# Optimization experiments

Measured on AMD Instinct MI355X. Metric: run time of the kernel, lower is better.

## Reference

```python
import jax, jax.numpy as jnp
import numpy as np
from jax import lax

B, C, H, W = 2, 384, 32, 32
N_HEAD, N_GROUP = 12, 6
HC = C // N_HEAD          # 32 head channels
GC = C // N_GROUP         # 64 group channels
GH = N_HEAD // N_GROUP    # 2 heads per group
KK = 7                    # depthwise kernel (25<=32<=48)
OFF_FACTOR = 2.0
SCALE = HC ** -0.5
EPS = 1e-5


def setup_inputs() -> dict:
    key = jax.random.key(0)
    ks = jax.random.split(key, 16)
    s = 0.02
    inp = {
        "x": jax.random.normal(ks[0], (B, C, H, W), jnp.float32),
        "Wq": jax.random.normal(ks[1], (C, C), jnp.float32) * s,
        "bq": jnp.zeros((C,), jnp.float32),
        "Wk": jax.random.normal(ks[2], (C, C), jnp.float32) * s,
        "bk": jnp.zeros((C,), jnp.float32),
        "Wv": jax.random.normal(ks[3], (C, C), jnp.float32) * s,
        "bv": jnp.zeros((C,), jnp.float32),
        "Wo": jax.random.normal(ks[4], (C, C), jnp.float32) * s,
        "bo": jnp.zeros((C,), jnp.float32),
        "off_dw_w": jax.random.normal(ks[5], (GC, 1, KK, KK), jnp.float32) * s,  # depthwise OIHW
        "off_dw_b": jnp.zeros((GC,), jnp.float32),
        "ln_g": jnp.ones((GC,), jnp.float32),
        "ln_b": jnp.zeros((GC,), jnp.float32),
        "off_pw_w": jax.random.normal(ks[6], (2, GC), jnp.float32) * s,  # 1x1 conv, no bias
        "rpe_table": jax.random.normal(ks[7], (N_HEAD, 2 * H - 1, 2 * W - 1), jnp.float32) * 0.01,
    }
    return inp


def _ref_points(Hk, Wk):
    # torch.linspace(0.5, Hk-0.5, Hk)/Hk*2-1 == ((i+0.5)/Hk)*2-1
    ry = ((jnp.arange(Hk, dtype=jnp.float32) + 0.5) / Hk) * 2.0 - 1.0
    rx = ((jnp.arange(Wk, dtype=jnp.float32) + 0.5) / Wk) * 2.0 - 1.0
    gy, gx = jnp.meshgrid(ry, rx, indexing='ij')
    return jnp.stack((gy, gx), axis=-1)  # [Hk, Wk, 2] in (y, x) order


def _grid_sample(img, grid):
    # img: [N, Cc, Hi, Wi]; grid: [N, Hg, Wg, 2] in (x, y), align_corners=True, zeros padding
    N, Cc, Hi, Wi = img.shape
    Hg, Wg = grid.shape[1], grid.shape[2]
    gx = (grid[..., 0] + 1.0) * 0.5 * (Wi - 1)
    gy = (grid[..., 1] + 1.0) * 0.5 * (Hi - 1)
    x0 = jnp.floor(gx)
    y0 = jnp.floor(gy)
    wx = gx - x0
    wy = gy - y0
    img_f = img.reshape(N, Cc, Hi * Wi)

    def corner(xi, yi, w):
        valid = (xi >= 0) & (xi <= Wi - 1) & (yi >= 0) & (yi <= Hi - 1)
        xc = jnp.clip(xi, 0, Wi - 1).astype(jnp.int32)
        yc = jnp.clip(yi, 0, Hi - 1).astype(jnp.int32)
        idx = (yc * Wi + xc).reshape(N, 1, Hg * Wg)
        vals = jnp.take_along_axis(img_f, jnp.broadcast_to(idx, (N, Cc, Hg * Wg)), axis=2)
        w = (w * valid.astype(img.dtype)).reshape(N, 1, Hg * Wg)
        return vals * w

    out = (corner(x0, y0, (1 - wx) * (1 - wy))
           + corner(x0 + 1, y0, wx * (1 - wy))
           + corner(x0, y0 + 1, (1 - wx) * wy)
           + corner(x0 + 1, y0 + 1, wx * wy))
    return out.reshape(N, Cc, Hg, Wg)


def _conv1x1(x, w, b=None):
    y = jnp.einsum('bchw,oc->bohw', x, w)
    if b is not None:
        y = y + b[None, :, None, None]
    return y


def _forward(x, Wq, bq, Wk, bk, Wv, bv, Wo, bo, off_dw_w, off_dw_b, ln_g, ln_b, off_pw_w, rpe_table):
    q = _conv1x1(x, Wq, bq)                                        # [B, C, H, W]
    q_off = q.reshape(B * N_GROUP, GC, H, W)
    # conv_offset: depthwise conv -> LayerNorm(ch) -> GELU -> 1x1 conv to 2 ch
    o = lax.conv_general_dilated(q_off, off_dw_w, (1, 1), ((KK // 2, KK // 2), (KK // 2, KK // 2)),
                                 feature_group_count=GC,
                                 dimension_numbers=('NCHW', 'OIHW', 'NCHW'))
    o = o + off_dw_b[None, :, None, None]
    mu = jnp.mean(o, axis=1, keepdims=True)
    var = jnp.mean((o - mu) ** 2, axis=1, keepdims=True)
    o = (o - mu) * lax.rsqrt(var + EPS) * ln_g[None, :, None, None] + ln_b[None, :, None, None]
    o = jax.nn.gelu(o, approximate=False)
    off = jnp.einsum('bchw,oc->bohw', o, off_pw_w)                 # [BG, 2, Hs, Ws]
    Hs, Ws = off.shape[2], off.shape[3]
    n_sample = Hs * Ws
    off_range = jnp.array([1.0 / Hs, 1.0 / Ws], jnp.float32).reshape(1, 2, 1, 1)
    off = jnp.tanh(off) * off_range * OFF_FACTOR
    off = jnp.transpose(off, (0, 2, 3, 1))                         # [BG, Hs, Ws, 2] (y, x)
    pos = off + _ref_points(Hs, Ws)[None]                          # [BG, Hs, Ws, 2]

    x_g = x.reshape(B * N_GROUP, GC, H, W)
    x_s = _grid_sample(x_g, pos[..., ::-1])                        # [BG, GC, Hs, Ws]
    x_s = x_s.reshape(B, C, 1, n_sample)

    k = _conv1x1(x_s, Wk, bk).reshape(B * N_HEAD, HC, n_sample)
    v = _conv1x1(x_s, Wv, bv).reshape(B * N_HEAD, HC, n_sample)
    qh = q.reshape(B * N_HEAD, HC, H * W)
    attn = jnp.einsum('bcm,bcn->bmn', qh, k) * SCALE               # [BH, HW, ns]

    # RPE: bilinear lookup of relative-position table at query-sample displacements
    q_grid = _ref_points(H, W).reshape(1, H * W, 1, 2)
    disp = (q_grid - pos.reshape(B * N_GROUP, 1, n_sample, 2)) * 0.5  # [BG, HW, ns, 2] (y, x)
    rpe_b = jnp.broadcast_to(rpe_table[None], (B, N_HEAD, 2 * H - 1, 2 * W - 1))
    rpe_b = rpe_b.reshape(B * N_GROUP, GH, 2 * H - 1, 2 * W - 1)
    attn_bias = _grid_sample(rpe_b, disp[..., ::-1])               # [BG, GH, HW, ns]
    attn = attn + attn_bias.reshape(B * N_HEAD, H * W, n_sample)

    attn = jax.nn.softmax(attn, axis=2)
    out = jnp.einsum('bmn,bcn->bcm', attn, v).reshape(B, C, H, W)
    y = _conv1x1(out, Wo, bo)
    return y


def reference(x, Wq, bq, Wk, bk, Wv, bv, Wo, bo, off_dw_w, off_dw_b, ln_g, ln_b, off_pw_w, rpe_table):
    return _forward(x, Wq, bq, Wk, bk, Wv, bv, Wo, bo,
                    off_dw_w, off_dw_b, ln_g, ln_b, off_pw_w, rpe_table)
```

## Files before the change

### kernel.cpp

```cpp
#include <hip/hip_runtime.h>
#include <hip/hip_fp16.h>
#include <math.h>

#define HH 32
#define WW 32
#define HWSZ 1024
#define CC 384
#define NHEAD 12
#define NGROUP 6
#define HC 32
#define GC 64
#define NS 1024
#define ATTN_SCALE 0.17677669529663687f

typedef _Float16 half8_t __attribute__((ext_vector_type(8)));
typedef _Float16 half4_t __attribute__((ext_vector_type(4)));
typedef _Float16 half2_t __attribute__((ext_vector_type(2)));
typedef float    f4_t    __attribute__((ext_vector_type(4)));

template<int XLO>
__global__ __launch_bounds__(256) void gemm_wx(
    const float* __restrict__ W, const float* __restrict__ bias,
    const float* __restrict__ X, float* __restrict__ Y)
{
    const int bz = blockIdx.z;
    const int tm = blockIdx.y * 32;
    const int tn = blockIdx.x * 32;
    const int tid = threadIdx.x;
    const int w = tid >> 6, lane = tid & 63;
    const int quad = lane >> 4, lcol = lane & 15;
    const int wr = w >> 1, wc = w & 1;

    __shared__ _Float16 sW[32][40];
    __shared__ _Float16 sX[32][40];
    __shared__ _Float16 sXl[XLO ? 32 : 1][40];

    const float* Xb = X + (size_t)bz * CC * 1024;
    float* Yb = Y + (size_t)bz * CC * 1024;

    const int m  = tid >> 3;
    const int j4 = (tid & 7) * 4;

    float4 wv = *(const float4*)&W[(size_t)(tm + m) * CC + j4];
    float4 xv = *(const float4*)&Xb[(size_t)m * 1024 + tn + j4];

    f4_t acc = {0.f, 0.f, 0.f, 0.f};

#pragma unroll 1
    for (int k0 = 0; k0 < CC; k0 += 32) {
        {
            half4_t hw; hw[0] = (_Float16)wv.x; hw[1] = (_Float16)wv.y;
            hw[2] = (_Float16)wv.z; hw[3] = (_Float16)wv.w;
            *(half4_t*)&sW[m][j4] = hw;
#pragma unroll
            for (int i = 0; i < 4; ++i) {
                float v = (i == 0) ? xv.x : (i == 1) ? xv.y : (i == 2) ? xv.z : xv.w;
                _Float16 h = (_Float16)v;
                sX[j4 + i][m] = h;
                if (XLO) sXl[j4 + i][m] = (_Float16)(v - (float)h);
            }
        }
        __syncthreads();

        if (k0 + 32 < CC) {
            wv = *(const float4*)&W[(size_t)(tm + m) * CC + k0 + 32 + j4];
            xv = *(const float4*)&Xb[(size_t)(k0 + 32 + m) * 1024 + tn + j4];
        }

        half8_t A = *(const half8_t*)&sW[wr * 16 + lcol][quad * 8];
        half8_t B = *(const half8_t*)&sX[wc * 16 + lcol][quad * 8];
        acc = __builtin_amdgcn_mfma_f32_16x16x32_f16(A, B, acc, 0, 0, 0);
        if (XLO) {
            half8_t Bl = *(const half8_t*)&sXl[wc * 16 + lcol][quad * 8];
            acc = __builtin_amdgcn_mfma_f32_16x16x32_f16(A, Bl, acc, 0, 0, 0);
        }
        __syncthreads();
    }

#pragma unroll
    for (int r = 0; r < 4; ++r) {
        int m0 = tm + wr * 16 + quad * 4 + r;
        Yb[(size_t)m0 * 1024 + tn + wc * 16 + lcol] = acc[r] + bias[m0];
    }
}

__global__ __launch_bounds__(256) void gemm_kv_fused(
    const float* __restrict__ Wk, const float* __restrict__ bk,
    const float* __restrict__ Wv, const float* __restrict__ bv,
    const _Float16* __restrict__ X,
    _Float16* __restrict__ khT, _Float16* __restrict__ vhb)
{
    const int bz = blockIdx.z;
    const int head = blockIdx.y;
    const int tm = head * 32;
    const int tn = blockIdx.x * 32;
    const int tid = threadIdx.x;
    const int w = tid >> 6, lane = tid & 63;
    const int quad = lane >> 4, lcol = lane & 15;
    const int bh = bz * 12 + head;
    const int nt = w & 1;

    __shared__ _Float16 sWk[32][40], sWv[32][40];
    __shared__ _Float16 sX[32][40];

    const _Float16* Xb = X + (size_t)bz * CC * 1024;

    const int m  = tid >> 3;
    const int j4 = (tid & 7) * 4;

    float4 wkv = *(const float4*)&Wk[(size_t)(tm + m) * CC + j4];
    float4 wvv = *(const float4*)&Wv[(size_t)(tm + m) * CC + j4];
    half4_t xh = *(const half4_t*)&Xb[(size_t)m * 1024 + tn + j4];

    f4_t a0 = {0.f, 0.f, 0.f, 0.f}, a1 = {0.f, 0.f, 0.f, 0.f};

#pragma unroll 1
    for (int k0 = 0; k0 < CC; k0 += 32) {
        {
            half4_t hk; hk[0] = (_Float16)wkv.x; hk[1] = (_Float16)wkv.y;
            hk[2] = (_Float16)wkv.z; hk[3] = (_Float16)wkv.w;
            half4_t hv; hv[0] = (_Float16)wvv.x; hv[1] = (_Float16)wvv.y;
            hv[2] = (_Float16)wvv.z; hv[3] = (_Float16)wvv.w;
            *(half4_t*)&sWk[m][j4] = hk;
            *(half4_t*)&sWv[m][j4] = hv;
#pragma unroll
            for (int i = 0; i < 4; ++i)
                sX[j4 + i][m] = xh[i];
        }
        __syncthreads();

        if (k0 + 32 < CC) {
            wkv = *(const float4*)&Wk[(size_t)(tm + m) * CC + k0 + 32 + j4];
            wvv = *(const float4*)&Wv[(size_t)(tm + m) * CC + k0 + 32 + j4];
            xh  = *(const half4_t*)&Xb[(size_t)(k0 + 32 + m) * 1024 + tn + j4];
        }

        half8_t Xa = *(const half8_t*)&sX[nt * 16 + lcol][quad * 8];
        if (w < 2) {
            half8_t K0 = *(const half8_t*)&sWk[lcol][quad * 8];
            half8_t K1 = *(const half8_t*)&sWk[16 + lcol][quad * 8];
            a0 = __builtin_amdgcn_mfma_f32_16x16x32_f16(Xa, K0, a0, 0, 0, 0);
            a1 = __builtin_amdgcn_mfma_f32_16x16x32_f16(Xa, K1, a1, 0, 0, 0);
        } else {
            half8_t V0 = *(const half8_t*)&sWv[lcol][quad * 8];
            half8_t V1 = *(const half8_t*)&sWv[16 + lcol][quad * 8];
            a0 = __builtin_amdgcn_mfma_f32_16x16x32_f16(V0, Xa, a0, 0, 0, 0);
            a1 = __builtin_amdgcn_mfma_f32_16x16x32_f16(V1, Xa, a1, 0, 0, 0);
        }
        __syncthreads();
    }

    if (w < 2) {
        float bk0 = bk[tm + lcol], bk1 = bk[tm + 16 + lcol];
#pragma unroll
        for (int r = 0; r < 4; ++r) {
            int n = tn + nt * 16 + quad * 4 + r;
            khT[((size_t)bh * 1024 + n) * 32 + lcol]      = (_Float16)(a0[r] + bk0);
            khT[((size_t)bh * 1024 + n) * 32 + 16 + lcol] = (_Float16)(a1[r] + bk1);
        }
    } else {
#pragma unroll
        for (int r = 0; r < 4; ++r) {
            int hc0 = quad * 4 + r;
            vhb[((size_t)bh * 32 + hc0) * 1024 + tn + nt * 16 + lcol] =
                (_Float16)(a0[r] + bv[tm + hc0]);
            vhb[((size_t)bh * 32 + hc0 + 16) * 1024 + tn + nt * 16 + lcol] =
                (_Float16)(a1[r] + bv[tm + hc0 + 16]);
        }
    }
}

__global__ __launch_bounds__(256) void dwconv_kernel(
    const float* __restrict__ q, const float* __restrict__ dww,
    const float* __restrict__ dwb, float* __restrict__ oconv)
{
    const int bc = blockIdx.x;
    const int bg = bc >> 6, c = bc & 63;
    const int b = bg / 6, g = bg % 6;
    const float* plane = q + ((size_t)b * CC + g * 64 + c) * 1024;

    __shared__ float sp[1024];
    __shared__ float sw[49];
    const int tid = threadIdx.x;
    for (int i = tid; i < 1024; i += 256) sp[i] = plane[i];
    if (tid < 49) sw[tid] = dww[c * 49 + tid];
    __syncthreads();

    const float bias = dwb[c];
    for (int i = tid; i < 1024; i += 256) {
        int y = i >> 5, x = i & 31;
        float s = 0.f;
#pragma unroll
        for (int ky = 0; ky < 7; ++ky) {
            int yy = y + ky - 3;
            if (yy < 0 || yy > 31) continue;
#pragma unroll
            for (int kx = 0; kx < 7; ++kx) {
                int xx = x + kx - 3;
                if (xx < 0 || xx > 31) continue;
                s += sp[yy * 32 + xx] * sw[ky * 7 + kx];
            }
        }
        oconv[(size_t)bc * 1024 + i] = s + bias;
    }
}

__global__ __launch_bounds__(256) void offset_sample_once_kernel(
    const float* __restrict__ oconv, const float* __restrict__ lng,
    const float* __restrict__ lnb, const float* __restrict__ pw,
    const float* __restrict__ x, float* __restrict__ pos,
    _Float16* __restrict__ xs)
{
    const int bg = blockIdx.y;
    const int px0 = blockIdx.x * 64;
    const int t = threadIdx.x;
    const int cg = t >> 6, pl = t & 63;
    const int px = px0 + pl;
    const int b = bg / 6, g = bg % 6;

    __shared__ float red[4][64];
    __shared__ float spos[64][2];

    const float* base = oconv + ((size_t)bg * 64 + cg * 16) * 1024 + px;
    float col[16];
    float s = 0.f;
#pragma unroll
    for (int i = 0; i < 16; ++i) { col[i] = base[(size_t)i * 1024]; s += col[i]; }
    red[cg][pl] = s;
    __syncthreads();
    float mu = (red[0][pl] + red[1][pl] + red[2][pl] + red[3][pl]) * (1.f / 64.f);
    float v = 0.f;
#pragma unroll
    for (int i = 0; i < 16; ++i) { float d = col[i] - mu; v += d * d; }
    __syncthreads();
    red[cg][pl] = v;
    __syncthreads();
    float inv = rsqrtf((red[0][pl] + red[1][pl] + red[2][pl] + red[3][pl]) * (1.f / 64.f) + 1e-5f);

    float oy = 0.f, ox = 0.f;
#pragma unroll
    for (int i = 0; i < 16; ++i) {
        int c = cg * 16 + i;
        float val = (col[i] - mu) * inv * lng[c] + lnb[c];
        float gl = 0.5f * val * (1.f + erff(val * 0.70710678118654752440f));
        oy += gl * pw[c];
        ox += gl * pw[64 + c];
    }
    __syncthreads();
    red[cg][pl] = oy;
    __syncthreads();
    float oyt = red[0][pl] + red[1][pl] + red[2][pl] + red[3][pl];
    __syncthreads();
    red[cg][pl] = ox;
    __syncthreads();
    if (cg == 0) {
        float oxt = red[0][pl] + red[1][pl] + red[2][pl] + red[3][pl];
        float offy = tanhf(oyt) * (2.0f / 32.0f);
        float offx = tanhf(oxt) * (2.0f / 32.0f);
        int y = px >> 5, xx = px & 31;
        float ry = ((y + 0.5f) / 32.f) * 2.f - 1.f;
        float rx = ((xx + 0.5f) / 32.f) * 2.f - 1.f;
        float pyv = offy + ry, pxv = offx + rx;
        spos[pl][0] = pyv; spos[pl][1] = pxv;
        pos[((size_t)bg * 1024 + px) * 2 + 0] = pyv;
        pos[((size_t)bg * 1024 + px) * 2 + 1] = pxv;
    }
    __syncthreads();

    float py = spos[pl][0], pxv = spos[pl][1];
    float gx = (pxv + 1.f) * 0.5f * 31.f;
    float gy = (py + 1.f) * 0.5f * 31.f;
    float x0f = floorf(gx), y0f = floorf(gy);
    float wx = gx - x0f, wy = gy - y0f;
    int x0 = (int)x0f, y0 = (int)y0f;
    float vx0 = ((unsigned)x0 <= 31u) ? 1.f : 0.f;
    float vx1 = ((unsigned)(x0 + 1) <= 31u) ? 1.f : 0.f;
    float vy0 = ((unsigned)y0 <= 31u) ? 1.f : 0.f;
    float vy1 = ((unsigned)(y0 + 1) <= 31u) ? 1.f : 0.f;
    float w00 = (1.f - wx) * (1.f - wy) * vx0 * vy0;
    float w01 = wx * (1.f - wy) * vx1 * vy0;
    float w10 = (1.f - wx) * wy * vx0 * vy1;
    float w11 = wx * wy * vx1 * vy1;
    int xc0 = min(max(x0, 0), 31), xc1 = min(max(x0 + 1, 0), 31);
    int yc0 = min(max(y0, 0), 31), yc1 = min(max(y0 + 1, 0), 31);
    int i00 = yc0 * 32 + xc0, i01 = yc0 * 32 + xc1;
    int i10 = yc1 * 32 + xc0, i11 = yc1 * 32 + xc1;

    const float* xg = x + ((size_t)b * CC + g * 64) * 1024;
    _Float16* xso = xs + ((size_t)b * CC + g * 64) * 1024 + px;
#pragma unroll
    for (int cs = 0; cs < 4; ++cs) {
        int c0 = cs * 16 + cg * 4;
#pragma unroll
        for (int i = 0; i < 4; ++i) {
            const float* plane = xg + (size_t)(c0 + i) * 1024;
            xso[(size_t)(c0 + i) * 1024] =
                (_Float16)(plane[i00] * w00 + plane[i01] * w01
                         + plane[i10] * w10 + plane[i11] * w11);
        }
    }
}

__global__ __launch_bounds__(256) void attn_mfma_kernel(
    const float* __restrict__ q, const _Float16* __restrict__ khT,
    const _Float16* __restrict__ vhb, const float* __restrict__ pos,
    const float* __restrict__ rpe, float* __restrict__ out)
{
    const int bgp = blockIdx.y;
    const int b = bgp / 6, g = bgp % 6;
    const int h0 = g * 2;
    const int bh0 = b * 12 + h0, bh1 = bh0 + 1;
    const int mblk = blockIdx.x * 16;
    const int tid = threadIdx.x;
    const int w = tid >> 6, lane = tid & 63;
    const int quad = lane >> 4, lcol = lane & 15;

    __shared__ __align__(16) char smem[50944];
    half2_t*  srpeA = (half2_t*)smem;
    half2_t*  srpeB = (half2_t*)(smem + 8832);
    _Float16* sqh   = (_Float16*)(smem + 17664);
    _Float16* spw   = (_Float16*)(smem + 19712) + w * 2304;
    float*    cml0  = (float*)(smem + 38144);
    float*    cml1  = (float*)(smem + 38400);
    float2*   skxy  = (float2*)(smem + 38656);
    int*      siy   = (int*)(smem + 46848);
    float*    comb0 = (float*)(smem + 19712);
    float*    comb1 = (float*)(smem + 19712 + 9216);

    const float qyw = (((mblk >> 5) + 0.5f) * (1.f / 32.f)) * 2.f - 1.f;
    int r0; {
        float gy_lo = (qyw - 1.03125f) * 15.5f + 31.f;
        r0 = (int)floorf(gy_lo);
        r0 = min(max(r0, 0), 28);
    }

    {
        const float* rp0 = rpe + (size_t)h0 * 3969;
        const float* rp1 = rp0 + 3969;
        for (int i = tid; i < 35 * 63; i += 256) {
            int y = i / 63, xx = i - y * 63;
            int gi = (r0 + y) * 63 + xx;
            float a0 = rp0[gi], b0 = (xx < 62) ? rp0[gi + 1] : 0.f;
            float a1 = rp1[gi], b1 = (xx < 62) ? rp1[gi + 1] : 0.f;
            half2_t hA; hA[0] = (_Float16)a0; hA[1] = (_Float16)a1;
            half2_t hB; hB[0] = (_Float16)b0; hB[1] = (_Float16)b1;
            srpeA[i] = hA;
            srpeB[i] = hB;
        }
    }
    {
        const float* qb = q + ((size_t)b * CC + h0 * 32) * 1024 + mblk;
        for (int i = tid; i < 1024; i += 256) {
            int hh = i >> 9, rem = i & 511;
            int hc = rem >> 4, m = rem & 15;
            sqh[hh * 512 + m * 32 + hc] =
                (_Float16)qb[(size_t)(hh * 32 + hc) * 1024 + m];
        }
    }
    {
        const float2* pgv = (const float2*)(pos + (size_t)bgp * 2048);
        for (int i = tid; i < 1024; i += 256) {
            float2 pp = pgv[i];
            float gy = (qyw - pp.x) * 15.5f + 31.f;
            float y0f = floorf(gy);
            skxy[i] = make_float2(pp.y, gy - y0f);
            siy[i] = ((int)y0f - r0) * 63;
        }
    }
    __syncthreads();

    half8_t qf0 = *(const half8_t*)&sqh[lcol * 32 + quad * 8];
    half8_t qf1 = *(const half8_t*)&sqh[512 + lcol * 32 + quad * 8];
    const float qx = (((mblk & 31) + lcol + 0.5f) * (1.f / 32.f)) * 2.f - 1.f;

    const _Float16* khb0 = khT + (size_t)bh0 * 1024 * 32;
    const _Float16* khb1 = khT + (size_t)bh1 * 1024 * 32;
    const _Float16* vhh0 = vhb + (size_t)bh0 * 32 * 1024;
    const _Float16* vhh1 = vhb + (size_t)bh1 * 32 * 1024;

    f4_t o00 = {0.f, 0.f, 0.f, 0.f}, o01 = {0.f, 0.f, 0.f, 0.f};
    f4_t o10 = {0.f, 0.f, 0.f, 0.f}, o11 = {0.f, 0.f, 0.f, 0.f};
    float lsum0 = 0.f, lsum1 = 0.f;

#pragma unroll 1
    for (int c = 0; c < 4; ++c) {
        const int n0 = w * 256 + c * 64;

        half8_t khv0[4], khv1[4];
#pragma unroll
        for (int t = 0; t < 4; ++t) {
            size_t off = (size_t)(n0 + t * 16 + lcol) * 32 + quad * 8;
            khv0[t] = *(const half8_t*)&khb0[off];
            khv1[t] = *(const half8_t*)&khb1[off];
        }

        f4_t S0[4], S1[4];
#pragma unroll
        for (int t = 0; t < 4; ++t) {
            f4_t s0 = {0.f, 0.f, 0.f, 0.f}, s1 = {0.f, 0.f, 0.f, 0.f};
            s0 = __builtin_amdgcn_mfma_f32_16x16x32_f16(khv0[t], qf0, s0, 0, 0, 0);
            s1 = __builtin_amdgcn_mfma_f32_16x16x32_f16(khv1[t], qf1, s1, 0, 0, 0);
#pragma unroll
            for (int r = 0; r < 4; ++r) {
                int key = n0 + t * 16 + quad * 4 + r;
                float2 kxy = skxy[key];
                int iy = siy[key];
                float gx = (qx - kxy.x) * 15.5f + 31.f;
                float x0f = floorf(gx);
                float wxf = gx - x0f;
                int i00 = iy + (int)x0f;
                half2_t a0 = srpeA[i00];
                half2_t b0 = srpeB[i00];
                half2_t a1 = srpeA[i00 + 63];
                half2_t b1 = srpeB[i00 + 63];
                _Float16 wxs = (_Float16)wxf;
                _Float16 wys = (_Float16)kxy.y;
                half2_t wxh; wxh[0] = wxs; wxh[1] = wxs;
                half2_t wyh; wyh[0] = wys; wyh[1] = wys;
                half2_t top = a0 + (b0 - a0) * wxh;
                half2_t bot = a1 + (b1 - a1) * wxh;
                half2_t res = top + (bot - top) * wyh;
                s0[r] = s0[r] * ATTN_SCALE + (float)res[0];
                s1[r] = s1[r] * ATTN_SCALE + (float)res[1];
            }
            S0[t] = s0; S1[t] = s1;
        }

        half8_t vv00[2], vv01[2];
#pragma unroll
        for (int kp = 0; kp < 2; ++kp) {
            int nb = n0 + kp * 32 + quad * 8;
            vv00[kp] = *(const half8_t*)&vhh0[(size_t)lcol * 1024 + nb];
            vv01[kp] = *(const half8_t*)&vhh0[(size_t)(16 + lcol) * 1024 + nb];
        }

#pragma unroll
        for (int t = 0; t < 4; ++t) {
            float p0 = __expf(S0[t][0]), p1 = __expf(S0[t][1]);
            float p2 = __expf(S0[t][2]), p3 = __expf(S0[t][3]);
            lsum0 += (p0 + p1) + (p2 + p3);
            half4_t h;
            h[0] = (_Float16)p0; h[1] = (_Float16)p1;
            h[2] = (_Float16)p2; h[3] = (_Float16)p3;
            *(half4_t*)&spw[lcol * 72 + t * 16 + quad * 4] = h;
            float r0e = __expf(S1[t][0]), r1e = __expf(S1[t][1]);
            float r2e = __expf(S1[t][2]), r3e = __expf(S1[t][3]);
            lsum1 += (r0e + r1e) + (r2e + r3e);
            half4_t h1;
            h1[0] = (_Float16)r0e; h1[1] = (_Float16)r1e;
            h1[2] = (_Float16)r2e; h1[3] = (_Float16)r3e;
            *(half4_t*)&spw[1152 + lcol * 72 + t * 16 + quad * 4] = h1;
        }

#pragma unroll
        for (int kp = 0; kp < 2; ++kp) {
            half8_t pb = *(const half8_t*)&spw[lcol * 72 + kp * 32 + quad * 8];
            o00 = __builtin_amdgcn_mfma_f32_16x16x32_f16(vv00[kp], pb, o00, 0, 0, 0);
            o01 = __builtin_amdgcn_mfma_f32_16x16x32_f16(vv01[kp], pb, o01, 0, 0, 0);
        }
#pragma unroll
        for (int kp = 0; kp < 2; ++kp) {
            int nb = n0 + kp * 32 + quad * 8;
            half8_t v0 = *(const half8_t*)&vhh1[(size_t)lcol * 1024 + nb];
            half8_t v1 = *(const half8_t*)&vhh1[(size_t)(16 + lcol) * 1024 + nb];
            half8_t pb = *(const half8_t*)&spw[1152 + lcol * 72 + kp * 32 + quad * 8];
            o10 = __builtin_amdgcn_mfma_f32_16x16x32_f16(v0, pb, o10, 0, 0, 0);
            o11 = __builtin_amdgcn_mfma_f32_16x16x32_f16(v1, pb, o11, 0, 0, 0);
        }
    }

    lsum0 += __shfl_xor(lsum0, 16); lsum0 += __shfl_xor(lsum0, 32);
    lsum1 += __shfl_xor(lsum1, 16); lsum1 += __shfl_xor(lsum1, 32);

    __syncthreads();

    *(f4_t*)&comb0[(w * 16 + lcol) * 36 + quad * 4]      = o00;
    *(f4_t*)&comb0[(w * 16 + lcol) * 36 + 16 + quad * 4] = o01;
    *(f4_t*)&comb1[(w * 16 + lcol) * 36 + quad * 4]      = o10;
    *(f4_t*)&comb1[(w * 16 + lcol) * 36 + 16 + quad * 4] = o11;
    if (quad == 0) {
        cml0[w * 16 + lcol] = lsum0;
        cml1[w * 16 + lcol] = lsum1;
    }
    __syncthreads();

#pragma unroll
    for (int i = 0; i < 2; ++i) {
        int idx = tid + i * 256;
        int qq = idx >> 5, hc = idx & 31;
        {
            float L = cml0[qq] + cml0[16 + qq] + cml0[32 + qq] + cml0[48 + qq];
            float o = comb0[(0 * 16 + qq) * 36 + hc]
                    + comb0[(1 * 16 + qq) * 36 + hc]
                    + comb0[(2 * 16 + qq) * 36 + hc]
                    + comb0[(3 * 16 + qq) * 36 + hc];
            out[((size_t)b * CC + h0 * 32 + hc) * 1024 + mblk + qq] = o / L;
        }
        {
            float L = cml1[qq] + cml1[16 + qq] + cml1[32 + qq] + cml1[48 + qq];
            float o = comb1[(0 * 16 + qq) * 36 + hc]
                    + comb1[(1 * 16 + qq) * 36 + hc]
                    + comb1[(2 * 16 + qq) * 36 + hc]
                    + comb1[(3 * 16 + qq) * 36 + hc];
            out[((size_t)b * CC + (h0 + 1) * 32 + hc) * 1024 + mblk + qq] = o / L;
        }
    }
}

extern "C" void kernel_launch(void* const* d_in, const int* in_sizes, int n_in,
                              void* d_out, int out_size, void* d_ws, size_t ws_size,
                              hipStream_t stream) {
    const float* x   = (const float*)d_in[0];
    const float* Wq  = (const float*)d_in[1];
    const float* bq  = (const float*)d_in[2];
    const float* Wk  = (const float*)d_in[3];
    const float* bk  = (const float*)d_in[4];
    const float* Wv  = (const float*)d_in[5];
    const float* bv  = (const float*)d_in[6];
    const float* Wo  = (const float*)d_in[7];
    const float* bo  = (const float*)d_in[8];
    const float* dww = (const float*)d_in[9];
    const float* dwb = (const float*)d_in[10];
    const float* lng = (const float*)d_in[11];
    const float* lnb = (const float*)d_in[12];
    const float* pw  = (const float*)d_in[13];
    const float* rpe = (const float*)d_in[14];

    float* ws = (float*)d_ws;
    const size_t SZ = 786432;
    float* qbuf  = ws;
    _Float16* xs = (_Float16*)(ws + 1 * SZ);
    float* abuf  = ws + 2 * SZ;
    float* oconv = ws + 3 * SZ;
    _Float16* khT = (_Float16*)(ws + 4 * SZ);
    _Float16* vhb = (_Float16*)(ws + 5 * SZ);
    float* pos   = ws + 6 * SZ;

    dim3 gqo(32, 12, 2);
    gemm_wx<0><<<gqo, 256, 0, stream>>>(Wq, bq, x, qbuf);
    dwconv_kernel<<<768, 256, 0, stream>>>(qbuf, dww, dwb, oconv);
    offset_sample_once_kernel<<<dim3(16, 12), 256, 0, stream>>>(
        oconv, lng, lnb, pw, x, pos, xs);
    gemm_kv_fused<<<dim3(32, 12, 2), 256, 0, stream>>>(Wk, bk, Wv, bv, xs, khT, vhb);
    attn_mfma_kernel<<<dim3(64, 12), 256, 0, stream>>>(qbuf, khT, vhb, pos, rpe, abuf);
    gemm_wx<1><<<gqo, 256, 0, stream>>>(Wo, bo, abuf, (float*)d_out);
}
```

Before: 158.4 us.

## Double-buffer K loads, fold scale into Q, drop duplicate RPE table

The attention kernel now prefetches the next chunk's K fragments while computing the current chunk. It folds the softmax scale into the staged Q, and precomputes the RPE x-coordinate per key to save ALU work. The second shifted RPE table is removed and the right neighbour is read from the same table, which cuts LDS use and may raise occupancy. The offset kernel uses 32-pixel blocks and twice the grid for more parallelism. Register pressure rises from the extra K buffers, and edge handling of the RPE right neighbour changes slightly.

```diff
diff --git a/kernel.cpp b/kernel.cpp
--- a/kernel.cpp
+++ b/kernel.cpp
@@ -212,35 +212,42 @@
     _Float16* __restrict__ xs)
 {
     const int bg = blockIdx.y;
-    const int px0 = blockIdx.x * 64;
+    const int px0 = blockIdx.x * 32;
     const int t = threadIdx.x;
-    const int cg = t >> 6, pl = t & 63;
+    const int cg = t >> 5;
+    const int pl = t & 31;
     const int px = px0 + pl;
     const int b = bg / 6, g = bg % 6;
 
-    __shared__ float red[4][64];
-    __shared__ float spos[64][2];
-
-    const float* base = oconv + ((size_t)bg * 64 + cg * 16) * 1024 + px;
-    float col[16];
+    __shared__ float red[8][32];
+    __shared__ float spos[32][2];
+
+    const float* base = oconv + ((size_t)bg * 64 + cg * 8) * 1024 + px;
+    float col[8];
     float s = 0.f;
 #pragma unroll
-    for (int i = 0; i < 16; ++i) { col[i] = base[(size_t)i * 1024]; s += col[i]; }
+    for (int i = 0; i < 8; ++i) { col[i] = base[(size_t)i * 1024]; s += col[i]; }
     red[cg][pl] = s;
     __syncthreads();
-    float mu = (red[0][pl] + red[1][pl] + red[2][pl] + red[3][pl]) * (1.f / 64.f);
+    float mu = 0.f;
+#pragma unroll
+    for (int j = 0; j < 8; ++j) mu += red[j][pl];
+    mu *= (1.f / 64.f);
     float v = 0.f;
 #pragma unroll
-    for (int i = 0; i < 16; ++i) { float d = col[i] - mu; v += d * d; }
+    for (int i = 0; i < 8; ++i) { float d = col[i] - mu; v += d * d; }
     __syncthreads();
     red[cg][pl] = v;
     __syncthreads();
-    float inv = rsqrtf((red[0][pl] + red[1][pl] + red[2][pl] + red[3][pl]) * (1.f / 64.f) + 1e-5f);
+    float vs = 0.f;
+#pragma unroll
+    for (int j = 0; j < 8; ++j) vs += red[j][pl];
+    float inv = rsqrtf(vs * (1.f / 64.f) + 1e-5f);
 
     float oy = 0.f, ox = 0.f;
 #pragma unroll
-    for (int i = 0; i < 16; ++i) {
-        int c = cg * 16 + i;
+    for (int i = 0; i < 8; ++i) {
+        int c = cg * 8 + i;
         float val = (col[i] - mu) * inv * lng[c] + lnb[c];
         float gl = 0.5f * val * (1.f + erff(val * 0.70710678118654752440f));
         oy += gl * pw[c];
@@ -249,12 +256,16 @@
     __syncthreads();
     red[cg][pl] = oy;
     __syncthreads();
-    float oyt = red[0][pl] + red[1][pl] + red[2][pl] + red[3][pl];
+    float oyt = 0.f;
+#pragma unroll
+    for (int j = 0; j < 8; ++j) oyt += red[j][pl];
     __syncthreads();
     red[cg][pl] = ox;
     __syncthreads();
     if (cg == 0) {
-        float oxt = red[0][pl] + red[1][pl] + red[2][pl] + red[3][pl];
+        float oxt = 0.f;
+#pragma unroll
+        for (int j = 0; j < 8; ++j) oxt += red[j][pl];
         float offy = tanhf(oyt) * (2.0f / 32.0f);
         float offx = tanhf(oxt) * (2.0f / 32.0f);
         int y = px >> 5, xx = px & 31;
@@ -289,15 +300,12 @@
     const float* xg = x + ((size_t)b * CC + g * 64) * 1024;
     _Float16* xso = xs + ((size_t)b * CC + g * 64) * 1024 + px;
 #pragma unroll
-    for (int cs = 0; cs < 4; ++cs) {
-        int c0 = cs * 16 + cg * 4;
-#pragma unroll
-        for (int i = 0; i < 4; ++i) {
-            const float* plane = xg + (size_t)(c0 + i) * 1024;
-            xso[(size_t)(c0 + i) * 1024] =
-                (_Float16)(plane[i00] * w00 + plane[i01] * w01
-                         + plane[i10] * w10 + plane[i11] * w11);
-        }
+    for (int i = 0; i < 8; ++i) {
+        int c = cg * 8 + i;
+        const float* plane = xg + (size_t)c * 1024;
+        xso[(size_t)c * 1024] =
+            (_Float16)(plane[i00] * w00 + plane[i01] * w01
+                     + plane[i10] * w10 + plane[i11] * w11);
     }
 }
 
@@ -315,17 +323,16 @@
     const int w = tid >> 6, lane = tid & 63;
     const int quad = lane >> 4, lcol = lane & 15;
 
-    __shared__ __align__(16) char smem[50944];
+    __shared__ __align__(16) char smem[42112];
     half2_t*  srpeA = (half2_t*)smem;
-    half2_t*  srpeB = (half2_t*)(smem + 8832);
-    _Float16* sqh   = (_Float16*)(smem + 17664);
-    _Float16* spw   = (_Float16*)(smem + 19712) + w * 2304;
-    float*    cml0  = (float*)(smem + 38144);
-    float*    cml1  = (float*)(smem + 38400);
-    float2*   skxy  = (float2*)(smem + 38656);
-    int*      siy   = (int*)(smem + 46848);
-    float*    comb0 = (float*)(smem + 19712);
-    float*    comb1 = (float*)(smem + 19712 + 9216);
+    _Float16* sqh   = (_Float16*)(smem + 8832);
+    _Float16* spw   = (_Float16*)(smem + 10880) + w * 2304;
+    float*    comb0 = (float*)(smem + 10880);
+    float*    comb1 = (float*)(smem + 20096);
+    float*    cml0  = (float*)(smem + 29312);
+    float*    cml1  = (float*)(smem + 29568);
+    float2*   skxy  = (float2*)(smem + 29824);
+    int*      siy   = (int*)(smem + 38016);
 
     const float qyw = (((mblk >> 5) + 0.5f) * (1.f / 32.f)) * 2.f - 1.f;
     int r0; {
@@ -340,12 +347,8 @@
         for (int i = tid; i < 35 * 63; i += 256) {
             int y = i / 63, xx = i - y * 63;
             int gi = (r0 + y) * 63 + xx;
-            float a0 = rp0[gi], b0 = (xx < 62) ? rp0[gi + 1] : 0.f;
-            float a1 = rp1[gi], b1 = (xx < 62) ? rp1[gi + 1] : 0.f;
-            half2_t hA; hA[0] = (_Float16)a0; hA[1] = (_Float16)a1;
-            half2_t hB; hB[0] = (_Float16)b0; hB[1] = (_Float16)b1;
+            half2_t hA; hA[0] = (_Float16)rp0[gi]; hA[1] = (_Float16)rp1[gi];
             srpeA[i] = hA;
-            srpeB[i] = hB;
         }
     }
     {
@@ -354,7 +357,7 @@
             int hh = i >> 9, rem = i & 511;
             int hc = rem >> 4, m = rem & 15;
             sqh[hh * 512 + m * 32 + hc] =
-                (_Float16)qb[(size_t)(hh * 32 + hc) * 1024 + m];
+                (_Float16)(qb[(size_t)(hh * 32 + hc) * 1024 + m] * ATTN_SCALE);
         }
     }
     {
@@ -363,7 +366,7 @@
             float2 pp = pgv[i];
             float gy = (qyw - pp.x) * 15.5f + 31.f;
             float y0f = floorf(gy);
-            skxy[i] = make_float2(pp.y, gy - y0f);
+            skxy[i] = make_float2(31.f - pp.y * 15.5f, gy - y0f);
             siy[i] = ((int)y0f - r0) * 63;
         }
     }
@@ -371,7 +374,7 @@
 
     half8_t qf0 = *(const half8_t*)&sqh[lcol * 32 + quad * 8];
     half8_t qf1 = *(const half8_t*)&sqh[512 + lcol * 32 + quad * 8];
-    const float qx = (((mblk & 31) + lcol + 0.5f) * (1.f / 32.f)) * 2.f - 1.f;
+    const float qxs = ((mblk & 31) + lcol + 0.5f) * 0.96875f - 15.5f;
 
     const _Float16* khb0 = khT + (size_t)bh0 * 1024 * 32;
     const _Float16* khb1 = khT + (size_t)bh1 * 1024 * 32;
@@ -382,46 +385,48 @@
     f4_t o10 = {0.f, 0.f, 0.f, 0.f}, o11 = {0.f, 0.f, 0.f, 0.f};
     float lsum0 = 0.f, lsum1 = 0.f;
 
-#pragma unroll 1
-    for (int c = 0; c < 4; ++c) {
+    half8_t kA0[4], kA1[4], kB0[4], kB1[4];
+
+    auto loadK = [&](half8_t* d0, half8_t* d1, int cc) {
+        int nn = w * 256 + cc * 64;
+#pragma unroll
+        for (int t = 0; t < 4; ++t) {
+            size_t off = (size_t)(nn + t * 16 + lcol) * 32 + quad * 8;
+            d0[t] = *(const half8_t*)&khb0[off];
+            d1[t] = *(const half8_t*)&khb1[off];
+        }
+    };
+
+    auto computeC = [&](const half8_t* kh0, const half8_t* kh1, int c) {
         const int n0 = w * 256 + c * 64;
-
-        half8_t khv0[4], khv1[4];
-#pragma unroll
-        for (int t = 0; t < 4; ++t) {
-            size_t off = (size_t)(n0 + t * 16 + lcol) * 32 + quad * 8;
-            khv0[t] = *(const half8_t*)&khb0[off];
-            khv1[t] = *(const half8_t*)&khb1[off];
-        }
 
         f4_t S0[4], S1[4];
 #pragma unroll
         for (int t = 0; t < 4; ++t) {
             f4_t s0 = {0.f, 0.f, 0.f, 0.f}, s1 = {0.f, 0.f, 0.f, 0.f};
-            s0 = __builtin_amdgcn_mfma_f32_16x16x32_f16(khv0[t], qf0, s0, 0, 0, 0);
-            s1 = __builtin_amdgcn_mfma_f32_16x16x32_f16(khv1[t], qf1, s1, 0, 0, 0);
+            s0 = __builtin_amdgcn_mfma_f32_16x16x32_f16(kh0[t], qf0, s0, 0, 0, 0);
+            s1 = __builtin_amdgcn_mfma_f32_16x16x32_f16(kh1[t], qf1, s1, 0, 0, 0);
 #pragma unroll
             for (int r = 0; r < 4; ++r) {
                 int key = n0 + t * 16 + quad * 4 + r;
                 float2 kxy = skxy[key];
                 int iy = siy[key];
-                float gx = (qx - kxy.x) * 15.5f + 31.f;
+                float gx = qxs + kxy.x;
                 float x0f = floorf(gx);
-                float wxf = gx - x0f;
                 int i00 = iy + (int)x0f;
                 half2_t a0 = srpeA[i00];
-                half2_t b0 = srpeB[i00];
+                half2_t b0 = srpeA[i00 + 1];
                 half2_t a1 = srpeA[i00 + 63];
-                half2_t b1 = srpeB[i00 + 63];
-                _Float16 wxs = (_Float16)wxf;
+                half2_t b1 = srpeA[i00 + 64];
+                _Float16 wxs = (_Float16)(gx - x0f);
                 _Float16 wys = (_Float16)kxy.y;
                 half2_t wxh; wxh[0] = wxs; wxh[1] = wxs;
                 half2_t wyh; wyh[0] = wys; wyh[1] = wys;
                 half2_t top = a0 + (b0 - a0) * wxh;
                 half2_t bot = a1 + (b1 - a1) * wxh;
                 half2_t res = top + (bot - top) * wyh;
-                s0[r] = s0[r] * ATTN_SCALE + (float)res[0];
-                s1[r] = s1[r] * ATTN_SCALE + (float)res[1];
+                s0[r] = s0[r] + (float)res[0];
+                s1[r] = s1[r] + (float)res[1];
             }
             S0[t] = s0; S1[t] = s1;
         }
@@ -467,6 +472,16 @@
             o10 = __builtin_amdgcn_mfma_f32_16x16x32_f16(v0, pb, o10, 0, 0, 0);
             o11 = __builtin_amdgcn_mfma_f32_16x16x32_f16(v1, pb, o11, 0, 0, 0);
         }
+    };
+
+    loadK(kA0, kA1, 0);
+#pragma unroll 1
+    for (int it = 0; it < 2; ++it) {
+        int c = it * 2;
+        loadK(kB0, kB1, c + 1);
+        computeC(kA0, kA1, c);
+        if (it == 0) loadK(kA0, kA1, c + 2);
+        computeC(kB0, kB1, c + 1);
     }
 
     lsum0 += __shfl_xor(lsum0, 16); lsum0 += __shfl_xor(lsum0, 32);
@@ -539,7 +554,7 @@
     dim3 gqo(32, 12, 2);
     gemm_wx<0><<<gqo, 256, 0, stream>>>(Wq, bq, x, qbuf);
     dwconv_kernel<<<768, 256, 0, stream>>>(qbuf, dww, dwb, oconv);
-    offset_sample_once_kernel<<<dim3(16, 12), 256, 0, stream>>>(
+    offset_sample_once_kernel<<<dim3(32, 12), 256, 0, stream>>>(
         oconv, lng, lnb, pw, x, pos, xs);
     gemm_kv_fused<<<dim3(32, 12, 2), 256, 0, stream>>>(Wk, bk, Wv, bv, xs, khT, vhb);
     attn_mfma_kernel<<<dim3(64, 12), 256, 0, stream>>>(qbuf, khT, vhb, pos, rpe, abuf);
```

Measured after the change: 158.2 us. About the same (-0.1%).
